# Performance work log

Hardware: AMD Instinct MI355X
Metric: run time of the kernel (lower is better)

Reference implementation:

```python
import jax, jax.numpy as jnp
import numpy as np

B = 8000      # graphs in batch
D = 128       # input_dim
H = 128       # hidden_dim
COUNTS = (2 + (np.arange(B) % 125)).astype(np.int32)   # nodes per graph in [2,126], sum = 512000
N = int(COUNTS.sum())
SEG = np.repeat(np.arange(B, dtype=np.int32), COUNTS)  # sorted graph id per node


def setup_inputs() -> dict:
    key = jax.random.key(0)
    k1, k2, k3, k4, k5 = jax.random.split(key, 5)
    return {
        "feats": jax.random.normal(k1, (N, D), dtype=jnp.float32),
        "W_u": jax.random.normal(k2, (D, H), dtype=jnp.float32) * 0.1,
        "W_v": jax.random.normal(k3, (D, H), dtype=jnp.float32) * 0.1,
        "b_v": jax.random.normal(k4, (H,), dtype=jnp.float32) * 0.1,
        "w_e": jax.random.normal(k5, (H, 1), dtype=jnp.float32) * 0.1,
        "seg": jnp.asarray(SEG),
        "counts": jnp.asarray(COUNTS),
    }


def reference(feats, W_u, W_v, b_v, w_e, seg, counts):
    nseg = counts.shape[0]
    fdt = feats.dtype
    # per-graph mean and max(|.|) over nodes, stacked interleaved as in the torch
    # code: rows of the table are [mean_g0, max_g0, mean_g1, max_g1, ...]
    ssum = jax.ops.segment_sum(feats, seg, num_segments=nseg, indices_are_sorted=True)
    mean = ssum / counts.astype(fdt)[:, None]                       # [B, D]
    mx = jax.ops.segment_max(jnp.abs(feats), seg, num_segments=nseg,
                             indices_are_sorted=True)               # [B, D]
    table = jnp.stack([mean, mx], axis=1).reshape(2 * nseg, -1)     # [2B, D]
    feat_u = feats @ W_u                                            # [N, H]
    # torch indexes the (2B)-row interleaved table with graph ids in [0,B)
    feat_v = (table @ W_v + b_v)[seg]                               # [N, H]
    e = jax.nn.sigmoid(feat_u + feat_v) @ w_e                       # [N, 1]
    # my_segment: exp only where nonzero, then segment-normalize (segment softmax)
    ee = jnp.where(e != 0, jnp.exp(e), e)
    den = jax.ops.segment_sum(ee, seg, num_segments=nseg, indices_are_sorted=True)[seg]
    alpha = ee / den                                                # [N, 1]
    # attention-weighted segment-sum pooling
    rst = jax.ops.segment_sum(feats * alpha, seg, num_segments=nseg,
                              indices_are_sorted=True)              # [B, D]
    return rst[:, None, :]                                          # [B, order=1, D]
```

## Files before the change

### kernel.cpp

```cpp
#include <hip/hip_runtime.h>
#include <hip/hip_bf16.h>
#include <math.h>

#define DD 128

typedef __attribute__((ext_vector_type(8))) short bf16x8;
typedef __attribute__((ext_vector_type(4))) float f32x4;

static __device__ __forceinline__ short f2bf(float x) {
    union { float f; unsigned u; } v; v.f = x;
    unsigned r = v.u + 0x7FFFu + ((v.u >> 16) & 1u);
    return (short)(r >> 16);
}
static __device__ __forceinline__ float bf2f(unsigned short h) {
    union { unsigned u; float f; } v; v.u = ((unsigned)h) << 16;
    return v.f;
}

__global__ void k0_combined(const int* __restrict__ counts, int* __restrict__ offs, int B,
                            const float* __restrict__ Wu, short* __restrict__ wuT)
{
    if (blockIdx.x == 0) {
        __shared__ int part[256];
        int t = threadIdx.x;
        int chunk = (B + 255) >> 8;
        int s = 0;
        for (int i = 0; i < chunk; ++i) {
            int idx = t * chunk + i;
            if (idx < B) s += counts[idx];
        }
        part[t] = s;
        __syncthreads();
        for (int off = 1; off < 256; off <<= 1) {
            int val = (t >= off) ? part[t - off] : 0;
            __syncthreads();
            part[t] += val;
            __syncthreads();
        }
        int run = (t > 0) ? part[t - 1] : 0;
        for (int i = 0; i < chunk; ++i) {
            int idx = t * chunk + i;
            if (idx < B) { offs[idx] = run; run += counts[idx]; }
        }
    } else {
        int idx = (blockIdx.x - 1) * 256 + threadIdx.x;
        int h = idx >> 7, k = idx & 127;
        wuT[(size_t)h * DD + k] = f2bf(Wu[(size_t)k * DD + h]);
    }
}

__global__ __launch_bounds__(256)
void k1_stats(const float* __restrict__ feats, const int* __restrict__ offs,
              const int* __restrict__ counts, float* __restrict__ mean,
              float* __restrict__ amax)
{
    int g = blockIdx.x;
    int s = offs[g], c = counts[g];
    int t = threadIdx.x;
    int col = (t & 31) * 4;
    int r0 = t >> 5;
    float4 sm = {0.f, 0.f, 0.f, 0.f};
    float4 mx = {0.f, 0.f, 0.f, 0.f};
    const float* base = feats + (size_t)s * DD + col;
    #pragma unroll 4
    for (int i = r0; i < c; i += 8) {
        float4 v = *(const float4*)(base + (size_t)i * DD);
        sm.x += v.x; sm.y += v.y; sm.z += v.z; sm.w += v.w;
        mx.x = fmaxf(mx.x, fabsf(v.x)); mx.y = fmaxf(mx.y, fabsf(v.y));
        mx.z = fmaxf(mx.z, fabsf(v.z)); mx.w = fmaxf(mx.w, fabsf(v.w));
    }
    __shared__ float ls[8][DD];
    __shared__ float lm[8][DD];
    *(float4*)&ls[r0][col] = sm;
    *(float4*)&lm[r0][col] = mx;
    __syncthreads();
    if (t < DD) {
        float ss = 0.f, mm = 0.f;
        #pragma unroll
        for (int r = 0; r < 8; ++r) {
            ss += ls[r][t];
            mm = fmaxf(mm, lm[r][t]);
        }
        mean[(size_t)g * DD + t] = ss / (float)c;
        amax[(size_t)g * DD + t] = mm;
    }
}

__global__ __launch_bounds__(128)
void k2_vtab(const float* __restrict__ mean, const float* __restrict__ amax,
             const float* __restrict__ Wv, const float* __restrict__ bv,
             float* __restrict__ vtab, int B)
{
    __shared__ float rows[16][DD];
    int g0 = blockIdx.x * 16;
    int h = threadIdx.x;
    for (int i = 0; i < 16; ++i) {
        int g = g0 + i;
        float val = 0.f;
        if (g < B) {
            int gg = g >> 1;
            const float* src = (g & 1) ? &amax[(size_t)gg * DD] : &mean[(size_t)gg * DD];
            val = src[h];
        }
        rows[i][h] = val;
    }
    __syncthreads();
    float acc[16];
    float bvh = bv[h];
    #pragma unroll
    for (int i = 0; i < 16; ++i) acc[i] = bvh;
    for (int d = 0; d < DD; d += 2) {
        float w0 = Wv[(size_t)d * DD + h];
        float w1 = Wv[(size_t)(d + 1) * DD + h];
        #pragma unroll
        for (int i = 0; i < 16; ++i) {
            float2 r = *(const float2*)&rows[i][d];
            acc[i] = fmaf(r.x, w0, acc[i]);
            acc[i] = fmaf(r.y, w1, acc[i]);
        }
    }
    #pragma unroll
    for (int i = 0; i < 16; ++i) {
        int g = g0 + i;
        if (g < B) vtab[(size_t)g * DD + h] = acc[i];
    }
}

__global__ __launch_bounds__(256, 4)
void kb_fused(const float* __restrict__ feats, const short* __restrict__ wuT,
              const float* __restrict__ vtab, const float* __restrict__ we,
              const int* __restrict__ offs, const int* __restrict__ counts,
              float* __restrict__ out)
{
    __shared__ short fe[128 * 128];
    __shared__ float eel[128];
    __shared__ float red[4][DD];
    __shared__ float dparts[4];

    const int g = blockIdx.x;
    const int s = offs[g], c = counts[g];
    const int t = threadIdx.x;
    const int w = t >> 6, lane = t & 63;
    const int l15 = lane & 15, kg = lane >> 4;
    char* feb = (char*)fe;

    const int cpad = (c + 15) & ~15;
    const int nch = cpad * 16;
    #pragma unroll 2
    for (int ch = t; ch < nch; ch += 256) {
        int row = ch >> 4, sub = ch & 15;
        union { bf16x8 v; short sh[8]; } u;
        if (row < c) {
            const float4* gp = (const float4*)(feats + (size_t)(s + row) * DD + sub * 8);
            float4 a = gp[0], b = gp[1];
            u.sh[0] = f2bf(a.x); u.sh[1] = f2bf(a.y); u.sh[2] = f2bf(a.z); u.sh[3] = f2bf(a.w);
            u.sh[4] = f2bf(b.x); u.sh[5] = f2bf(b.y); u.sh[6] = f2bf(b.z); u.sh[7] = f2bf(b.w);
        } else {
            u.v = (bf16x8){0, 0, 0, 0, 0, 0, 0, 0};
        }
        *(bf16x8*)(feb + row * 256 + ((sub * 16) ^ ((row & 7) << 4))) = u.v;
    }
    __syncthreads();

    float wv[8], vgv[8];
    #pragma unroll
    for (int ht = 0; ht < 8; ++ht) {
        wv[ht]  = we[l15 + ht * 16];
        vgv[ht] = vtab[(size_t)g * DD + l15 + ht * 16];
    }

    #pragma unroll
    for (int p = 0; p < 2; ++p) {
        const int tb = (w + p * 4) * 16;
        if (tb < c) {
            bf16x8 af[4];
            #pragma unroll
            for (int ks = 0; ks < 4; ++ks)
                af[ks] = *(const bf16x8*)(feb + (tb + l15) * 256 +
                                          ((ks * 64 + kg * 16) ^ ((l15 & 7) << 4)));
            f32x4 acc[8];
            #pragma unroll
            for (int ht = 0; ht < 8; ++ht) acc[ht] = (f32x4){0.f, 0.f, 0.f, 0.f};
            #pragma unroll
            for (int ks = 0; ks < 4; ++ks) {
                #pragma unroll
                for (int ht = 0; ht < 8; ++ht) {
                    bf16x8 bfr = *(const bf16x8*)(wuT + (size_t)(l15 + ht * 16) * DD + ks * 32 + kg * 8);
                    acc[ht] = __builtin_amdgcn_mfma_f32_16x16x32_bf16(af[ks], bfr, acc[ht], 0, 0, 0);
                }
            }
            #pragma unroll
            for (int r = 0; r < 4; ++r) {
                int node = tb + kg * 4 + r;
                float pp = 0.f;
                #pragma unroll
                for (int ht = 0; ht < 8; ++ht) {
                    float x = acc[ht][r] + vgv[ht];
                    float sg = 1.f / (1.f + __expf(-x));
                    pp = fmaf(sg, wv[ht], pp);
                }
                pp += __shfl_xor(pp, 1);
                pp += __shfl_xor(pp, 2);
                pp += __shfl_xor(pp, 4);
                pp += __shfl_xor(pp, 8);
                if (l15 == 0 && node < c)
                    eel[node] = (pp != 0.f) ? __expf(pp) : pp;
            }
        }
    }
    __syncthreads();

    {
        float px = 0.f, py = 0.f, dw = 0.f;
        #pragma unroll 4
        for (int i = w; i < c; i += 4) {
            unsigned pv = *(const unsigned*)(feb + i * 256 + ((lane * 4) ^ ((i & 7) << 4)));
            float wi = eel[i];
            dw += wi;
            px = fmaf(bf2f((unsigned short)(pv & 0xffffu)), wi, px);
            py = fmaf(bf2f((unsigned short)(pv >> 16)), wi, py);
        }
        red[w][lane * 2]     = px;
        red[w][lane * 2 + 1] = py;
        if (lane == 0) dparts[w] = dw;
    }
    __syncthreads();

    if (t < DD) {
        float den = (dparts[0] + dparts[1]) + (dparts[2] + dparts[3]);
        float a2 = (red[0][t] + red[1][t]) + (red[2][t] + red[3][t]);
        out[(size_t)g * DD + t] = a2 / den;
    }
}

extern "C" void kernel_launch(void* const* d_in, const int* in_sizes, int n_in,
                              void* d_out, int out_size, void* d_ws, size_t ws_size,
                              hipStream_t stream)
{
    const float* feats  = (const float*)d_in[0];
    const float* Wu     = (const float*)d_in[1];
    const float* Wv     = (const float*)d_in[2];
    const float* bv     = (const float*)d_in[3];
    const float* we     = (const float*)d_in[4];
    const int*   counts = (const int*)d_in[6];
    const int B = in_sizes[6];

    char* w = (char*)d_ws;
    int*   offs = (int*)w;    w += ((size_t)B * sizeof(int) + 255) & ~(size_t)255;
    float* mean = (float*)w;  w += (size_t)B * DD * sizeof(float);
    float* amax = (float*)w;  w += (size_t)B * DD * sizeof(float);
    float* vtab = (float*)w;  w += (size_t)B * DD * sizeof(float);
    short* wuT  = (short*)w;  w += (size_t)DD * DD * sizeof(short);

    k0_combined<<<65, 256, 0, stream>>>(counts, offs, B, Wu, wuT);
    k1_stats<<<B, 256, 0, stream>>>(feats, offs, counts, mean, amax);
    k2_vtab<<<(B + 15) / 16, 128, 0, stream>>>(mean, amax, Wv, bv, vtab, B);
    kb_fused<<<B, 256, 0, stream>>>(feats, wuT, vtab, we, offs, counts, (float*)d_out);
}
```

Measured before the change: 250.3 us.

## Tile fused attention kernel over fixed 128-node blocks with partial combine

Replaces the one-block-per-graph fused attention kernel with one that processes fixed 128-node tiles across graph boundaries, using the node-to-graph index to look up per-graph bias rows. Each tile writes per-graph partial weighted sums and denominators into two slots, and a new combine kernel merges them and normalizes. This removes the padding waste and load imbalance from graphs with varying, often small node counts. In exchange it adds a serial segment scan per tile, an extra kernel launch, and partial-buffer traffic, and it relies on each graph spanning at most two tiles.

```diff
diff --git a/kernel.cpp b/kernel.cpp
--- a/kernel.cpp
+++ b/kernel.cpp
@@ -127,31 +127,32 @@
 }
 
 __global__ __launch_bounds__(256, 4)
-void kb_fused(const float* __restrict__ feats, const short* __restrict__ wuT,
-              const float* __restrict__ vtab, const float* __restrict__ we,
-              const int* __restrict__ offs, const int* __restrict__ counts,
-              float* __restrict__ out)
-{
-    __shared__ short fe[128 * 128];
+void kc_flat(const float* __restrict__ feats, const short* __restrict__ wuT,
+             const float* __restrict__ vtab, const float* __restrict__ we,
+             const int* __restrict__ seg, const int* __restrict__ offs,
+             float* __restrict__ partial, float* __restrict__ dens, int N)
+{
+    __shared__ short fe[128 * DD];
     __shared__ float eel[128];
-    __shared__ float red[4][DD];
-    __shared__ float dparts[4];
-
-    const int g = blockIdx.x;
-    const int s = offs[g], c = counts[g];
+    __shared__ int   segl[128];
+    char* feb = (char*)fe;
     const int t = threadIdx.x;
-    const int w = t >> 6, lane = t & 63;
-    const int l15 = lane & 15, kg = lane >> 4;
-    char* feb = (char*)fe;
-
-    const int cpad = (c + 15) & ~15;
-    const int nch = cpad * 16;
-    #pragma unroll 2
-    for (int ch = t; ch < nch; ch += 256) {
+    const int bid = blockIdx.x;
+    const int n0 = bid << 7;
+
+    if (t < 128) {
+        int n = n0 + t;
+        segl[t] = seg[(n < N) ? n : (N - 1)];
+    }
+
+    #pragma unroll
+    for (int it = 0; it < 8; ++it) {
+        int ch = it * 256 + t;
         int row = ch >> 4, sub = ch & 15;
+        int n = n0 + row;
         union { bf16x8 v; short sh[8]; } u;
-        if (row < c) {
-            const float4* gp = (const float4*)(feats + (size_t)(s + row) * DD + sub * 8);
+        if (n < N) {
+            const float4* gp = (const float4*)(feats + (size_t)n * DD + sub * 8);
             float4 a = gp[0], b = gp[1];
             u.sh[0] = f2bf(a.x); u.sh[1] = f2bf(a.y); u.sh[2] = f2bf(a.z); u.sh[3] = f2bf(a.w);
             u.sh[4] = f2bf(b.x); u.sh[5] = f2bf(b.y); u.sh[6] = f2bf(b.z); u.sh[7] = f2bf(b.w);
@@ -162,75 +163,98 @@
     }
     __syncthreads();
 
-    float wv[8], vgv[8];
-    #pragma unroll
-    for (int ht = 0; ht < 8; ++ht) {
-        wv[ht]  = we[l15 + ht * 16];
-        vgv[ht] = vtab[(size_t)g * DD + l15 + ht * 16];
-    }
+    const int w = t >> 6, lane = t & 63;
+    const int l15 = lane & 15, kg = lane >> 4;
+
+    float wv[8];
+    #pragma unroll
+    for (int ht = 0; ht < 8; ++ht) wv[ht] = we[l15 + ht * 16];
 
     #pragma unroll
     for (int p = 0; p < 2; ++p) {
         const int tb = (w + p * 4) * 16;
-        if (tb < c) {
-            bf16x8 af[4];
+        bf16x8 af[4];
+        #pragma unroll
+        for (int ks = 0; ks < 4; ++ks)
+            af[ks] = *(const bf16x8*)(feb + (tb + l15) * 256 +
+                                      (((ks * 4 + kg) * 16) ^ ((l15 & 7) << 4)));
+        f32x4 acc[8];
+        #pragma unroll
+        for (int ht = 0; ht < 8; ++ht) acc[ht] = (f32x4){0.f, 0.f, 0.f, 0.f};
+        #pragma unroll
+        for (int ks = 0; ks < 4; ++ks) {
             #pragma unroll
-            for (int ks = 0; ks < 4; ++ks)
-                af[ks] = *(const bf16x8*)(feb + (tb + l15) * 256 +
-                                          ((ks * 64 + kg * 16) ^ ((l15 & 7) << 4)));
-            f32x4 acc[8];
+            for (int ht = 0; ht < 8; ++ht) {
+                bf16x8 bfr = *(const bf16x8*)(wuT + (size_t)(l15 + ht * 16) * DD + ks * 32 + kg * 8);
+                acc[ht] = __builtin_amdgcn_mfma_f32_16x16x32_bf16(af[ks], bfr, acc[ht], 0, 0, 0);
+            }
+        }
+        #pragma unroll
+        for (int r = 0; r < 4; ++r) {
+            int node = tb + kg * 4 + r;
+            int gn = segl[node];
+            const float* vg = vtab + (size_t)gn * DD + l15;
+            float pp = 0.f;
             #pragma unroll
-            for (int ht = 0; ht < 8; ++ht) acc[ht] = (f32x4){0.f, 0.f, 0.f, 0.f};
-            #pragma unroll
-            for (int ks = 0; ks < 4; ++ks) {
-                #pragma unroll
-                for (int ht = 0; ht < 8; ++ht) {
-                    bf16x8 bfr = *(const bf16x8*)(wuT + (size_t)(l15 + ht * 16) * DD + ks * 32 + kg * 8);
-                    acc[ht] = __builtin_amdgcn_mfma_f32_16x16x32_bf16(af[ks], bfr, acc[ht], 0, 0, 0);
-                }
-            }
-            #pragma unroll
-            for (int r = 0; r < 4; ++r) {
-                int node = tb + kg * 4 + r;
-                float pp = 0.f;
-                #pragma unroll
-                for (int ht = 0; ht < 8; ++ht) {
-                    float x = acc[ht][r] + vgv[ht];
-                    float sg = 1.f / (1.f + __expf(-x));
-                    pp = fmaf(sg, wv[ht], pp);
-                }
-                pp += __shfl_xor(pp, 1);
-                pp += __shfl_xor(pp, 2);
-                pp += __shfl_xor(pp, 4);
-                pp += __shfl_xor(pp, 8);
-                if (l15 == 0 && node < c)
-                    eel[node] = (pp != 0.f) ? __expf(pp) : pp;
-            }
-        }
-    }
-    __syncthreads();
-
-    {
-        float px = 0.f, py = 0.f, dw = 0.f;
-        #pragma unroll 4
-        for (int i = w; i < c; i += 4) {
-            unsigned pv = *(const unsigned*)(feb + i * 256 + ((lane * 4) ^ ((i & 7) << 4)));
+            for (int ht = 0; ht < 8; ++ht) {
+                float x = acc[ht][r] + vg[ht * 16];
+                float sg = 1.f / (1.f + __expf(-x));
+                pp = fmaf(sg, wv[ht], pp);
+            }
+            pp += __shfl_xor(pp, 1);
+            pp += __shfl_xor(pp, 2);
+            pp += __shfl_xor(pp, 4);
+            pp += __shfl_xor(pp, 8);
+            if (l15 == 0)
+                eel[node] = (n0 + node < N) ? ((pp != 0.f) ? __expf(pp) : pp) : 0.f;
+        }
+    }
+    __syncthreads();
+
+    if (t <= 64) {
+        const bool isden = (t == 64);
+        int cur = segl[0];
+        float ax = 0.f, ay = 0.f;
+        for (int i = 0; i < 128; ++i) {
+            int sgi = segl[i];
+            if (sgi != cur) {
+                int slot = ((offs[cur] >> 7) == bid) ? 0 : 1;
+                if (isden) dens[cur * 2 + slot] = ax;
+                else *(float2*)&partial[(size_t)(cur * 2 + slot) * DD + t * 2] = make_float2(ax, ay);
+                ax = 0.f; ay = 0.f; cur = sgi;
+            }
             float wi = eel[i];
-            dw += wi;
-            px = fmaf(bf2f((unsigned short)(pv & 0xffffu)), wi, px);
-            py = fmaf(bf2f((unsigned short)(pv >> 16)), wi, py);
-        }
-        red[w][lane * 2]     = px;
-        red[w][lane * 2 + 1] = py;
-        if (lane == 0) dparts[w] = dw;
-    }
-    __syncthreads();
-
-    if (t < DD) {
-        float den = (dparts[0] + dparts[1]) + (dparts[2] + dparts[3]);
-        float a2 = (red[0][t] + red[1][t]) + (red[2][t] + red[3][t]);
-        out[(size_t)g * DD + t] = a2 / den;
-    }
+            if (isden) {
+                ax += wi;
+            } else {
+                unsigned pv = *(const unsigned*)(feb + i * 256 + ((t * 4) ^ ((i & 7) << 4)));
+                ax = fmaf(bf2f((unsigned short)(pv & 0xffffu)), wi, ax);
+                ay = fmaf(bf2f((unsigned short)(pv >> 16)), wi, ay);
+            }
+        }
+        int slot = ((offs[cur] >> 7) == bid) ? 0 : 1;
+        if (isden) dens[cur * 2 + slot] = ax;
+        else *(float2*)&partial[(size_t)(cur * 2 + slot) * DD + t * 2] = make_float2(ax, ay);
+    }
+}
+
+__global__ __launch_bounds__(256)
+void kd_combine(const float* __restrict__ partial, const float* __restrict__ dens,
+                const int* __restrict__ offs, const int* __restrict__ counts,
+                float* __restrict__ out, int B)
+{
+    int g = blockIdx.x * 2 + (threadIdx.x >> 7);
+    int d = threadIdx.x & 127;
+    if (g >= B) return;
+    int off = offs[g], c = counts[g];
+    int b0 = off >> 7, b1 = (off + c - 1) >> 7;
+    float v = partial[(size_t)(g * 2) * DD + d];
+    float den = dens[g * 2];
+    if (b1 != b0) {
+        v += partial[(size_t)(g * 2 + 1) * DD + d];
+        den += dens[g * 2 + 1];
+    }
+    out[(size_t)g * DD + d] = v / den;
 }
 
 extern "C" void kernel_launch(void* const* d_in, const int* in_sizes, int n_in,
@@ -242,7 +266,9 @@
     const float* Wv     = (const float*)d_in[2];
     const float* bv     = (const float*)d_in[3];
     const float* we     = (const float*)d_in[4];
+    const int*   seg    = (const int*)d_in[5];
     const int*   counts = (const int*)d_in[6];
+    const int N = in_sizes[0] / DD;
     const int B = in_sizes[6];
 
     char* w = (char*)d_ws;
@@ -251,9 +277,14 @@
     float* amax = (float*)w;  w += (size_t)B * DD * sizeof(float);
     float* vtab = (float*)w;  w += (size_t)B * DD * sizeof(float);
     short* wuT  = (short*)w;  w += (size_t)DD * DD * sizeof(short);
+    float* dens = (float*)w;  w += (size_t)B * 2 * sizeof(float);
+    float* partial = mean;
 
     k0_combined<<<65, 256, 0, stream>>>(counts, offs, B, Wu, wuT);
     k1_stats<<<B, 256, 0, stream>>>(feats, offs, counts, mean, amax);
     k2_vtab<<<(B + 15) / 16, 128, 0, stream>>>(mean, amax, Wv, bv, vtab, B);
-    kb_fused<<<B, 256, 0, stream>>>(feats, wuT, vtab, we, offs, counts, (float*)d_out);
-}
+
+    const int blocks = (N + 127) / 128;
+    kc_flat<<<blocks, 256, 0, stream>>>(feats, wuT, vtab, we, seg, offs, partial, dens, N);
+    kd_combine<<<(B + 1) / 2, 256, 0, stream>>>(partial, dens, offs, counts, (float*)d_out, B);
+}
```

Result: slower. 335.9 us (+34.2%).
